# Kernel tuning notes

Hardware: AMD Instinct MI355X
Metric: run time of the kernel (lower is better)

## Reference

```python
import jax, jax.numpy as jnp
import numpy as np

B, S, D, H = 2, 2048, 1024, 16
DK = D // H

def setup_inputs() -> dict:
    key = jax.random.key(0)
    ks = jax.random.split(key, 12)
    scale = 1.0 / np.sqrt(D)
    inp = {
        'q_in': jax.random.normal(ks[0], (B, S, D), jnp.float32),
        'k_in': jax.random.normal(ks[1], (B, S, D), jnp.float32),
        'v_in': jax.random.normal(ks[2], (B, S, D), jnp.float32),
        'mask': jax.random.randint(ks[3], (B, 1, 1, S), 0, 2, jnp.int32),
        'w_q': jax.random.normal(ks[4], (D, D), jnp.float32) * scale,
        'b_q': jnp.zeros((D,), jnp.float32),
        'w_k': jax.random.normal(ks[5], (D, D), jnp.float32) * scale,
        'b_k': jnp.zeros((D,), jnp.float32),
        'w_v': jax.random.normal(ks[6], (D, D), jnp.float32) * scale,
        'b_v': jnp.zeros((D,), jnp.float32),
        'w_o': jax.random.normal(ks[7], (D, D), jnp.float32) * scale,
        'b_o': jnp.zeros((D,), jnp.float32),
    }
    return inp

def _split_heads(x):
    # [B, S, D] -> [B, H, S, DK]
    return x.reshape(B, S, H, DK).transpose(0, 2, 1, 3)

def reference(q_in, k_in, v_in, mask, w_q, b_q, w_k, b_k, w_v, b_v, w_o, b_o):
    q = _split_heads(q_in @ w_q.T + b_q)
    k = _split_heads(k_in @ w_k.T + b_k)
    v = _split_heads(v_in @ w_v.T + b_v)
    scores = jnp.einsum('bhqd,bhkd->bhqk', q, k) / jnp.sqrt(jnp.float32(DK))
    scores = jnp.where(mask == 0, jnp.float32(-1e9), scores)
    attn = jax.nn.softmax(scores, axis=-1)
    ctx = jnp.einsum('bhqk,bhkd->bhqd', attn, v)
    ctx = ctx.transpose(0, 2, 1, 3).reshape(B, S, D)
    return ctx @ w_o.T + b_o
```

## Files before the change

kernel.cpp:

```cpp
#include <hip/hip_runtime.h>
#include <math.h>

#define Bn 2
#define Sn 2048
#define Dn 1024
#define Hn 16
#define DKn 64
#define Mn (Bn*Sn)

typedef __bf16 bf16;
typedef __attribute__((ext_vector_type(8))) __bf16 bf16x8;
typedef __attribute__((ext_vector_type(4))) __bf16 bf16x4;
typedef __attribute__((ext_vector_type(4))) float f32x4;

__device__ inline f32x4 mfma16(bf16x8 a, bf16x8 b, f32x4 c) {
    return __builtin_amdgcn_mfma_f32_16x16x32_bf16(a, b, c, 0, 0, 0);
}

typedef __attribute__((address_space(3))) void lds_t;
typedef const __attribute__((address_space(1))) void gbl_t;
__device__ __forceinline__ void glds16(const void* g, void* l) {
    __builtin_amdgcn_global_load_lds((gbl_t*)g, (lds_t*)l, 16, 0, 0);
}

__global__ __launch_bounds__(256)
void conv3(const float* __restrict__ s0, const float* __restrict__ s1,
           const float* __restrict__ s2, bf16* __restrict__ d0,
           bf16* __restrict__ d1, bf16* __restrict__ d2)
{
    const float* s = blockIdx.y == 0 ? s0 : blockIdx.y == 1 ? s1 : s2;
    bf16*       d = blockIdx.y == 0 ? d0 : blockIdx.y == 1 ? d1 : d2;
    int i = (blockIdx.x * 256 + threadIdx.x) * 8;
    float4 a = *(const float4*)(s + i);
    float4 b = *(const float4*)(s + i + 4);
    bf16x8 o;
    o[0]=(bf16)a.x; o[1]=(bf16)a.y; o[2]=(bf16)a.z; o[3]=(bf16)a.w;
    o[4]=(bf16)b.x; o[5]=(bf16)b.y; o[6]=(bf16)b.z; o[7]=(bf16)b.w;
    *(bf16x8*)(d + i) = o;
}

__global__ __launch_bounds__(256)
void conv_w(const float* __restrict__ s0, const float* __restrict__ s1,
            const float* __restrict__ s2, const float* __restrict__ s3,
            bf16* __restrict__ d0, bf16* __restrict__ d1,
            bf16* __restrict__ d2, bf16* __restrict__ d3)
{
    const float* s = blockIdx.y == 0 ? s0 : blockIdx.y == 1 ? s1 :
                     blockIdx.y == 2 ? s2 : s3;
    bf16*       d = blockIdx.y == 0 ? d0 : blockIdx.y == 1 ? d1 :
                     blockIdx.y == 2 ? d2 : d3;
    int i = (blockIdx.x * 256 + threadIdx.x) * 8;
    float4 a = *(const float4*)(s + i);
    float4 b = *(const float4*)(s + i + 4);
    bf16x8 o;
    o[0]=(bf16)a.x; o[1]=(bf16)a.y; o[2]=(bf16)a.z; o[3]=(bf16)a.w;
    o[4]=(bf16)b.x; o[5]=(bf16)b.y; o[6]=(bf16)b.z; o[7]=(bf16)b.w;
    *(bf16x8*)(d + i) = o;
}

__global__ __launch_bounds__(64)
void mask_scan(const int* __restrict__ mask, int* __restrict__ inv,
               int* __restrict__ cnt)
{
    const int b    = blockIdx.x;
    const int lane = threadIdx.x;
    const int* mb  = mask + b * Sn;
    int loc[32];
    int c = 0;
    #pragma unroll
    for (int e = 0; e < 32; ++e) {
        loc[e] = (mb[lane * 32 + e] != 0) ? 1 : 0;
        c += loc[e];
    }
    int pre = c;
    #pragma unroll
    for (int off = 1; off < 64; off <<= 1) {
        int v = __shfl_up(pre, off);
        if (lane >= off) pre += v;
    }
    int excl  = pre - c;
    int total = __shfl(pre, 63);
    int un = excl;
    int ms = lane * 32 - excl;
    #pragma unroll
    for (int e = 0; e < 32; ++e) {
        int s = lane * 32 + e;
        if (loc[e]) { inv[b * Sn + un] = s;           ++un; }
        else        { inv[b * Sn + total + ms] = s;   ++ms; }
    }
    if (lane == 63) cnt[b] = total;
}

__global__ __launch_bounds__(256)
void gemm_proj(const bf16* __restrict__ Aq, const bf16* __restrict__ Ak,
               const bf16* __restrict__ Av, const bf16* __restrict__ Wq,
               const bf16* __restrict__ Wk, const bf16* __restrict__ Wv,
               const float* __restrict__ bq, const float* __restrict__ bk,
               const float* __restrict__ bv, const int* __restrict__ inv,
               const int* __restrict__ cnt,
               bf16* __restrict__ Cq, bf16* __restrict__ Ck, bf16* __restrict__ Cv)
{
    __shared__ bf16 As[128][32];
    __shared__ bf16 Ws_[128][32];

    const int bid = blockIdx.x;
    const int l   = (bid & 7) * 96 + (bid >> 3);
    const int z   = l >> 8;
    const int rem = l & 255;
    const int mt  = rem >> 3;
    const int n0  = (rem & 7) * 128;
    const int m0  = mt * 128;
    const int bb  = mt >> 4;
    const int s0  = (mt & 15) * 128;

    if (z >= 1) {
        int eff = cnt[bb];
        if (eff == 0) eff = Sn;
        if (s0 >= eff) return;
    }

    const bf16*  A    = z == 0 ? Aq : z == 1 ? Ak : Av;
    const bf16*  W    = z == 0 ? Wq : z == 1 ? Wk : Wv;
    const float* bias = z == 0 ? bq : z == 1 ? bk : bv;
    bf16*        C    = z == 0 ? Cq : z == 1 ? Ck : Cv;

    const int tid = threadIdx.x;
    const int w4 = tid >> 6, ln = tid & 63;
    const int p = ln & 15, g = ln >> 4;
    const int wr = w4 >> 1, wc = w4 & 1;

    const int arow = w4 * 32 + (ln >> 2);
    const int acol = (ln & 3) * 8;

    int row0, row1;
    if (z == 0) { row0 = m0 + arow; row1 = m0 + arow + 16; }
    else {
        row0 = bb * Sn + inv[bb * Sn + s0 + arow];
        row1 = bb * Sn + inv[bb * Sn + s0 + arow + 16];
    }
    const bf16* ga0 = A + (size_t)row0 * Dn + acol;
    const bf16* ga1 = A + (size_t)row1 * Dn + acol;
    const bf16* gw  = W + (size_t)(n0 + arow) * Dn + acol;

    f32x4 acc[4][4];
    #pragma unroll
    for (int mi = 0; mi < 4; ++mi)
        #pragma unroll
        for (int ni = 0; ni < 4; ++ni) acc[mi][ni] = (f32x4){0.f,0.f,0.f,0.f};

    for (int k0 = 0; k0 < Dn; k0 += 32) {
        __syncthreads();
        glds16(ga0 + k0,          &As [w4*32     ][0]);
        glds16(ga1 + k0,          &As [w4*32 + 16][0]);
        glds16(gw  + k0,          &Ws_[w4*32     ][0]);
        glds16(gw  + k0 + 16*Dn,  &Ws_[w4*32 + 16][0]);
        __syncthreads();

        bf16x8 af[4], bfr[4];
        #pragma unroll
        for (int mi = 0; mi < 4; ++mi)
            af[mi] = *(const bf16x8*)&As[wr*64 + mi*16 + p][g*8];
        #pragma unroll
        for (int ni = 0; ni < 4; ++ni)
            bfr[ni] = *(const bf16x8*)&Ws_[wc*64 + ni*16 + p][g*8];
        #pragma unroll
        for (int mi = 0; mi < 4; ++mi)
            #pragma unroll
            for (int ni = 0; ni < 4; ++ni)
                acc[mi][ni] = mfma16(af[mi], bfr[ni], acc[mi][ni]);
    }

    if (z == 0) {
        const float osc = 0.18033688011112042f;
        #pragma unroll
        for (int ni = 0; ni < 4; ++ni) {
            int n = n0 + wc*64 + ni*16 + p;
            int h = n >> 6, dk = n & (DKn - 1);
            float bv = bias[n];
            #pragma unroll
            for (int mi = 0; mi < 4; ++mi)
                #pragma unroll
                for (int r = 0; r < 4; ++r) {
                    int m = m0 + wr*64 + mi*16 + 4*g + r;
                    int b = m >> 11, s = m & (Sn - 1);
                    C[(((size_t)(b*Hn + h)*Sn + s)*DKn) + dk] =
                        (bf16)((acc[mi][ni][r] + bv) * osc);
                }
        }
    } else if (z == 1) {
        #pragma unroll
        for (int ni = 0; ni < 4; ++ni) {
            int n = n0 + wc*64 + ni*16 + p;
            int h = n >> 6, dk = n & (DKn - 1);
            float bv = bias[n];
            #pragma unroll
            for (int mi = 0; mi < 4; ++mi)
                #pragma unroll
                for (int r = 0; r < 4; ++r) {
                    int jj = s0 + wr*64 + mi*16 + 4*g + r;
                    C[(((size_t)(bb*Hn + h)*Sn + jj)*DKn) + dk] =
                        (bf16)(acc[mi][ni][r] + bv);
                }
        }
    } else {
        #pragma unroll
        for (int ni = 0; ni < 4; ++ni) {
            int n = n0 + wc*64 + ni*16 + p;
            int h = n >> 6, dk = n & (DKn - 1);
            float bv = bias[n];
            #pragma unroll
            for (int mi = 0; mi < 4; ++mi)
                #pragma unroll
                for (int r = 0; r < 4; ++r) {
                    int jj = s0 + wr*64 + mi*16 + 4*g + r;
                    C[(((size_t)(bb*Hn + h)*DKn + dk)*Sn) + jj] =
                        (bf16)(acc[mi][ni][r] + bv);
                }
        }
    }
}

__global__ __launch_bounds__(256)
void gemm_out(const bf16* __restrict__ A, const bf16* __restrict__ W,
              const float* __restrict__ bias, float* __restrict__ C)
{
    __shared__ bf16 As[128][32];
    __shared__ bf16 Ws_[64][32];

    const int bid = blockIdx.x;
    const int l   = (bid & 7) * 64 + (bid >> 3);
    const int m0  = (l >> 4) * 128;
    const int n0  = (l & 15) * 64;

    const int tid = threadIdx.x;
    const int w4 = tid >> 6, ln = tid & 63;
    const int p = ln & 15, g = ln >> 4;
    const int wr = w4 >> 1, wc = w4 & 1;

    const int arow = w4 * 32 + (ln >> 2);
    const int acol = (ln & 3) * 8;
    const bf16* ga = A + (size_t)(m0 + arow) * Dn + acol;
    const bf16* gw = W + (size_t)(n0 + w4*16 + (ln >> 2)) * Dn + acol;

    f32x4 acc[4][2];
    #pragma unroll
    for (int mi = 0; mi < 4; ++mi)
        #pragma unroll
        for (int ni = 0; ni < 2; ++ni) acc[mi][ni] = (f32x4){0.f,0.f,0.f,0.f};

    for (int k0 = 0; k0 < Dn; k0 += 32) {
        __syncthreads();
        glds16(ga + k0,          &As [w4*32     ][0]);
        glds16(ga + k0 + 16*Dn,  &As [w4*32 + 16][0]);
        glds16(gw + k0,          &Ws_[w4*16     ][0]);
        __syncthreads();

        bf16x8 af[4], bfr[2];
        #pragma unroll
        for (int mi = 0; mi < 4; ++mi)
            af[mi] = *(const bf16x8*)&As[wr*64 + mi*16 + p][g*8];
        #pragma unroll
        for (int ni = 0; ni < 2; ++ni)
            bfr[ni] = *(const bf16x8*)&Ws_[wc*32 + ni*16 + p][g*8];
        #pragma unroll
        for (int mi = 0; mi < 4; ++mi)
            #pragma unroll
            for (int ni = 0; ni < 2; ++ni)
                acc[mi][ni] = mfma16(af[mi], bfr[ni], acc[mi][ni]);
    }

    #pragma unroll
    for (int ni = 0; ni < 2; ++ni) {
        int n = n0 + wc*32 + ni*16 + p;
        float bv = bias[n];
        #pragma unroll
        for (int mi = 0; mi < 4; ++mi)
            #pragma unroll
            for (int r = 0; r < 4; ++r) {
                int m = m0 + wr*64 + mi*16 + 4*g + r;
                C[(size_t)m * Dn + n] = acc[mi][ni][r] + bv;
            }
    }
}

__global__ __launch_bounds__(512)
void attn_mfma(const bf16* __restrict__ Q, const bf16* __restrict__ K,
               const bf16* __restrict__ Vt, const int* __restrict__ cnt,
               bf16* __restrict__ ctx)
{
    __shared__ bf16 Ks[2][64][64];
    __shared__ bf16 Vs[2][64][64];
    __shared__ bf16 Ps[8][16][72];

    const int tid  = threadIdx.x;
    const int lane = tid & 63;
    const int w    = tid >> 6;
    const int g    = lane >> 4;
    const int p    = lane & 15;
    const int bh   = blockIdx.y;
    const int b    = bh >> 4;
    const int h    = bh & 15;
    const int q0   = blockIdx.x * 128;

    const int  cntb = cnt[b];
    const bool unif = (cntb == 0);
    const int  nt   = unif ? (Sn / 64) : ((cntb + 63) >> 6);

    const bf16* Qb = Q  + (size_t)bh * Sn * DKn;
    const bf16* Kb = K  + (size_t)bh * Sn * DKn;
    const bf16* Vb = Vt + (size_t)bh * DKn * Sn;

    const int sr   = lane >> 3;
    const int scol = 8 * ((lane & 7) ^ sr);
    const int drow = w * 8 + sr;
    const int swzk = (p & 7) << 3;
    const bf16* gK = Kb + (size_t)drow * DKn + scol;
    const bf16* gV = Vb + (size_t)drow * Sn  + scol;

    bf16x8 aq0, aq1;
    {
        const bf16* qrow = Qb + (size_t)(q0 + w*16 + p) * DKn + 8*g;
        aq0 = *(const bf16x8*)(qrow);
        aq1 = *(const bf16x8*)(qrow + 32);
    }

    f32x4 o[4];
    #pragma unroll
    for (int dt = 0; dt < 4; ++dt) o[dt] = (f32x4){0.f,0.f,0.f,0.f};
    float lq = 0.f;

    glds16(gK, &Ks[0][w*8][0]);
    glds16(gV, &Vs[0][w*8][0]);
    __syncthreads();

    int bf = 0;
    for (int kt = 0; kt < nt; ++kt) {
        if (kt + 1 < nt) {
            glds16(gK + (size_t)(kt+1)*64*DKn, &Ks[bf^1][w*8][0]);
            glds16(gV + (size_t)(kt+1)*64,     &Vs[bf^1][w*8][0]);
        }

        const bool tail = (!unif) && (kt == nt - 1);
        const int  rem  = cntb - (kt << 6);

        #pragma unroll
        for (int t = 0; t < 4; ++t) {
            f32x4 z = (f32x4){0.f,0.f,0.f,0.f};
            bf16x8 k0 = *(const bf16x8*)&Ks[bf][16*t + p][(8*g)      ^ swzk];
            bf16x8 k1 = *(const bf16x8*)&Ks[bf][16*t + p][(8*g + 32) ^ swzk];
            z = mfma16(k0, aq0, z);
            z = mfma16(k1, aq1, z);
            bf16x4 pk;
            if (unif) {
                pk[0] = (bf16)1.f; pk[1] = (bf16)1.f;
                pk[2] = (bf16)1.f; pk[3] = (bf16)1.f;
                lq += 4.f;
            } else if (tail) {
                int kb = 16*t + 4*g;
                pk[0] = (bf16)(kb + 0 < rem ? exp2f(z[0]) : 0.f);
                pk[1] = (bf16)(kb + 1 < rem ? exp2f(z[1]) : 0.f);
                pk[2] = (bf16)(kb + 2 < rem ? exp2f(z[2]) : 0.f);
                pk[3] = (bf16)(kb + 3 < rem ? exp2f(z[3]) : 0.f);
                lq += (float)pk[0] + (float)pk[1] + (float)pk[2] + (float)pk[3];
            } else {
                pk[0] = (bf16)exp2f(z[0]);
                pk[1] = (bf16)exp2f(z[1]);
                pk[2] = (bf16)exp2f(z[2]);
                pk[3] = (bf16)exp2f(z[3]);
                lq += (float)pk[0] + (float)pk[1] + (float)pk[2] + (float)pk[3];
            }
            *(bf16x4*)&Ps[w][p][16*t + 4*g] = pk;
        }

        bf16x8 pa0 = *(const bf16x8*)&Ps[w][p][8*g];
        bf16x8 pa1 = *(const bf16x8*)&Ps[w][p][32 + 8*g];
        #pragma unroll
        for (int dt = 0; dt < 4; ++dt) {
            bf16x8 v0 = *(const bf16x8*)&Vs[bf][16*dt + p][(8*g)      ^ swzk];
            bf16x8 v1 = *(const bf16x8*)&Vs[bf][16*dt + p][(8*g + 32) ^ swzk];
            o[dt] = mfma16(pa0, v0, o[dt]);
            o[dt] = mfma16(pa1, v1, o[dt]);
        }

        __syncthreads();
        bf ^= 1;
    }

    lq += __shfl_xor(lq, 16);
    lq += __shfl_xor(lq, 32);
    float ld[4];
    #pragma unroll
    for (int r = 0; r < 4; ++r) ld[r] = __shfl(lq, 4*g + r);

    #pragma unroll
    for (int dt = 0; dt < 4; ++dt)
        #pragma unroll
        for (int r = 0; r < 4; ++r) {
            int s_ = q0 + w*16 + 4*g + r;
            ctx[(size_t)(b*Sn + s_) * Dn + h*64 + 16*dt + p] =
                (bf16)(o[dt][r] / ld[r]);
        }
}

extern "C" void kernel_launch(void* const* d_in, const int* in_sizes, int n_in,
                              void* d_out, int out_size, void* d_ws, size_t ws_size,
                              hipStream_t stream) {
    const float* q_in = (const float*)d_in[0];
    const float* k_in = (const float*)d_in[1];
    const float* v_in = (const float*)d_in[2];
    const int*   mask = (const int*)  d_in[3];
    const float* w_q  = (const float*)d_in[4];
    const float* b_q  = (const float*)d_in[5];
    const float* w_k  = (const float*)d_in[6];
    const float* b_k  = (const float*)d_in[7];
    const float* w_v  = (const float*)d_in[8];
    const float* b_v  = (const float*)d_in[9];
    const float* w_o  = (const float*)d_in[10];
    const float* b_o  = (const float*)d_in[11];

    char* ws = (char*)d_ws;
    bf16* Abf_q = (bf16*)(ws);
    bf16* Abf_k = (bf16*)(ws + 8388608);
    bf16* Abf_v = (bf16*)(ws + 16777216);
    bf16* ctx   = (bf16*)(ws);
    bf16* Qh    = (bf16*)(ws + 25165824);
    bf16* Kh    = (bf16*)(ws + 33554432);
    bf16* Vt    = (bf16*)(ws + 41943040);
    bf16* Wbf_q = (bf16*)(ws + 50331648);
    bf16* Wbf_k = (bf16*)(ws + 52428800);
    bf16* Wbf_v = (bf16*)(ws + 54525952);
    bf16* Wbf_o = (bf16*)(ws + 56623104);
    int*  inv   = (int*) (ws + 58720256);
    int*  cntb  = (int*) (ws + 58736640);

    dim3 blk(256);
    conv3<<<dim3(2048, 3), blk, 0, stream>>>(q_in, k_in, v_in, Abf_q, Abf_k, Abf_v);
    conv_w<<<dim3(512, 4), blk, 0, stream>>>(w_q, w_k, w_v, w_o,
                                             Wbf_q, Wbf_k, Wbf_v, Wbf_o);
    mask_scan<<<dim3(Bn), dim3(64), 0, stream>>>(mask, inv, cntb);

    gemm_proj<<<dim3(768), blk, 0, stream>>>(
        Abf_q, Abf_k, Abf_v, Wbf_q, Wbf_k, Wbf_v, b_q, b_k, b_v, inv, cntb,
        Qh, Kh, Vt);

    attn_mfma<<<dim3(Sn/128, Bn*Hn), dim3(512), 0, stream>>>(Qh, Kh, Vt, cntb, ctx);

    gemm_out<<<dim3(512), blk, 0, stream>>>(ctx, Wbf_o, b_o, (float*)d_out);
}
```

Measured before the change: 125.2 us.

## Fuse prep kernels into one launch and use K=64 swizzled LDS tiles in GEMMs

The three preprocessing kernels (activation conversion, weight conversion, mask scan) are merged into a single launch, removing two kernel launches and their gaps. Both projection GEMMs now stage 64-wide K slices per iteration instead of 32, halving the number of barrier pairs per K loop. An XOR swizzle on the 16-byte column chunk is added to spread LDS accesses across banks. The doubled LDS footprint per block may reduce occupancy, and the mask-scan blocks leave most of their threads idle.

```diff
diff --git a/kernel.cpp b/kernel.cpp
--- a/kernel.cpp
+++ b/kernel.cpp
@@ -24,71 +24,65 @@
 }
 
 __global__ __launch_bounds__(256)
-void conv3(const float* __restrict__ s0, const float* __restrict__ s1,
-           const float* __restrict__ s2, bf16* __restrict__ d0,
-           bf16* __restrict__ d1, bf16* __restrict__ d2)
+void prep(const float* __restrict__ q_in, const float* __restrict__ k_in,
+          const float* __restrict__ v_in, const float* __restrict__ w_q,
+          const float* __restrict__ w_k, const float* __restrict__ w_v,
+          const float* __restrict__ w_o, const int* __restrict__ mask,
+          bf16* __restrict__ Aq, bf16* __restrict__ Ak, bf16* __restrict__ Av,
+          bf16* __restrict__ Wq, bf16* __restrict__ Wk, bf16* __restrict__ Wv,
+          bf16* __restrict__ Wo, int* __restrict__ inv, int* __restrict__ cnt)
 {
-    const float* s = blockIdx.y == 0 ? s0 : blockIdx.y == 1 ? s1 : s2;
-    bf16*       d = blockIdx.y == 0 ? d0 : blockIdx.y == 1 ? d1 : d2;
-    int i = (blockIdx.x * 256 + threadIdx.x) * 8;
-    float4 a = *(const float4*)(s + i);
-    float4 b = *(const float4*)(s + i + 4);
-    bf16x8 o;
-    o[0]=(bf16)a.x; o[1]=(bf16)a.y; o[2]=(bf16)a.z; o[3]=(bf16)a.w;
-    o[4]=(bf16)b.x; o[5]=(bf16)b.y; o[6]=(bf16)b.z; o[7]=(bf16)b.w;
-    *(bf16x8*)(d + i) = o;
-}
-
-__global__ __launch_bounds__(256)
-void conv_w(const float* __restrict__ s0, const float* __restrict__ s1,
-            const float* __restrict__ s2, const float* __restrict__ s3,
-            bf16* __restrict__ d0, bf16* __restrict__ d1,
-            bf16* __restrict__ d2, bf16* __restrict__ d3)
-{
-    const float* s = blockIdx.y == 0 ? s0 : blockIdx.y == 1 ? s1 :
-                     blockIdx.y == 2 ? s2 : s3;
-    bf16*       d = blockIdx.y == 0 ? d0 : blockIdx.y == 1 ? d1 :
-                     blockIdx.y == 2 ? d2 : d3;
-    int i = (blockIdx.x * 256 + threadIdx.x) * 8;
-    float4 a = *(const float4*)(s + i);
-    float4 b = *(const float4*)(s + i + 4);
-    bf16x8 o;
-    o[0]=(bf16)a.x; o[1]=(bf16)a.y; o[2]=(bf16)a.z; o[3]=(bf16)a.w;
-    o[4]=(bf16)b.x; o[5]=(bf16)b.y; o[6]=(bf16)b.z; o[7]=(bf16)b.w;
-    *(bf16x8*)(d + i) = o;
-}
-
-__global__ __launch_bounds__(64)
-void mask_scan(const int* __restrict__ mask, int* __restrict__ inv,
-               int* __restrict__ cnt)
-{
-    const int b    = blockIdx.x;
-    const int lane = threadIdx.x;
-    const int* mb  = mask + b * Sn;
-    int loc[32];
-    int c = 0;
-    #pragma unroll
-    for (int e = 0; e < 32; ++e) {
-        loc[e] = (mb[lane * 32 + e] != 0) ? 1 : 0;
-        c += loc[e];
-    }
-    int pre = c;
-    #pragma unroll
-    for (int off = 1; off < 64; off <<= 1) {
-        int v = __shfl_up(pre, off);
-        if (lane >= off) pre += v;
-    }
-    int excl  = pre - c;
-    int total = __shfl(pre, 63);
-    int un = excl;
-    int ms = lane * 32 - excl;
-    #pragma unroll
-    for (int e = 0; e < 32; ++e) {
-        int s = lane * 32 + e;
-        if (loc[e]) { inv[b * Sn + un] = s;           ++un; }
-        else        { inv[b * Sn + total + ms] = s;   ++ms; }
-    }
-    if (lane == 63) cnt[b] = total;
+    const int bid = blockIdx.x;
+    if (bid < 8192) {
+        const float* s; bf16* d; int i;
+        if (bid < 6144) {
+            int y = bid / 2048, x = bid - y * 2048;
+            s = y == 0 ? q_in : y == 1 ? k_in : v_in;
+            d = y == 0 ? Aq   : y == 1 ? Ak   : Av;
+            i = (x * 256 + threadIdx.x) * 8;
+        } else {
+            int r = bid - 6144;
+            int y = r / 512, x = r - y * 512;
+            s = y == 0 ? w_q : y == 1 ? w_k : y == 2 ? w_v : w_o;
+            d = y == 0 ? Wq  : y == 1 ? Wk  : y == 2 ? Wv  : Wo;
+            i = (x * 256 + threadIdx.x) * 8;
+        }
+        float4 a = *(const float4*)(s + i);
+        float4 b = *(const float4*)(s + i + 4);
+        bf16x8 o;
+        o[0]=(bf16)a.x; o[1]=(bf16)a.y; o[2]=(bf16)a.z; o[3]=(bf16)a.w;
+        o[4]=(bf16)b.x; o[5]=(bf16)b.y; o[6]=(bf16)b.z; o[7]=(bf16)b.w;
+        *(bf16x8*)(d + i) = o;
+    } else {
+        if (threadIdx.x >= 64) return;
+        const int b    = bid - 8192;
+        const int lane = threadIdx.x;
+        const int* mb  = mask + b * Sn;
+        int loc[32];
+        int c = 0;
+        #pragma unroll
+        for (int e = 0; e < 32; ++e) {
+            loc[e] = (mb[lane * 32 + e] != 0) ? 1 : 0;
+            c += loc[e];
+        }
+        int pre = c;
+        #pragma unroll
+        for (int off = 1; off < 64; off <<= 1) {
+            int v = __shfl_up(pre, off);
+            if (lane >= off) pre += v;
+        }
+        int excl  = pre - c;
+        int total = __shfl(pre, 63);
+        int un = excl;
+        int ms = lane * 32 - excl;
+        #pragma unroll
+        for (int e = 0; e < 32; ++e) {
+            int s = lane * 32 + e;
+            if (loc[e]) { inv[b * Sn + un] = s;           ++un; }
+            else        { inv[b * Sn + total + ms] = s;   ++ms; }
+        }
+        if (lane == 63) cnt[b] = total;
+    }
 }
 
 __global__ __launch_bounds__(256)
@@ -100,8 +94,8 @@
                const int* __restrict__ cnt,
                bf16* __restrict__ Cq, bf16* __restrict__ Ck, bf16* __restrict__ Cv)
 {
-    __shared__ bf16 As[128][32];
-    __shared__ bf16 Ws_[128][32];
+    __shared__ bf16 As[128][64];
+    __shared__ bf16 Ws_[128][64];
 
     const int bid = blockIdx.x;
     const int l   = (bid & 7) * 96 + (bid >> 3);
@@ -129,18 +123,21 @@
     const int p = ln & 15, g = ln >> 4;
     const int wr = w4 >> 1, wc = w4 & 1;
 
-    const int arow = w4 * 32 + (ln >> 2);
-    const int acol = (ln & 3) * 8;
-
-    int row0, row1;
-    if (z == 0) { row0 = m0 + arow; row1 = m0 + arow + 16; }
-    else {
-        row0 = bb * Sn + inv[bb * Sn + s0 + arow];
-        row1 = bb * Sn + inv[bb * Sn + s0 + arow + 16];
-    }
-    const bf16* ga0 = A + (size_t)row0 * Dn + acol;
-    const bf16* ga1 = A + (size_t)row1 * Dn + acol;
-    const bf16* gw  = W + (size_t)(n0 + arow) * Dn + acol;
+    const int lr   = ln >> 3;
+    const int scol = 8 * ((ln & 7) ^ lr);
+    const int sw   = p & 7;
+
+    const bf16* ga[4];
+    const bf16* gw[4];
+    #pragma unroll
+    for (int i = 0; i < 4; ++i) {
+        int lrow = w4*32 + i*8 + lr;
+        int row;
+        if (z == 0) row = m0 + lrow;
+        else        row = bb * Sn + inv[bb * Sn + s0 + lrow];
+        ga[i] = A + (size_t)row * Dn + scol;
+        gw[i] = W + (size_t)(n0 + lrow) * Dn + scol;
+    }
 
     f32x4 acc[4][4];
     #pragma unroll
@@ -148,26 +145,32 @@
         #pragma unroll
         for (int ni = 0; ni < 4; ++ni) acc[mi][ni] = (f32x4){0.f,0.f,0.f,0.f};
 
-    for (int k0 = 0; k0 < Dn; k0 += 32) {
+    for (int k0 = 0; k0 < Dn; k0 += 64) {
         __syncthreads();
-        glds16(ga0 + k0,          &As [w4*32     ][0]);
-        glds16(ga1 + k0,          &As [w4*32 + 16][0]);
-        glds16(gw  + k0,          &Ws_[w4*32     ][0]);
-        glds16(gw  + k0 + 16*Dn,  &Ws_[w4*32 + 16][0]);
+        #pragma unroll
+        for (int i = 0; i < 4; ++i) {
+            glds16(ga[i] + k0, &As [w4*32 + i*8][0]);
+            glds16(gw[i] + k0, &Ws_[w4*32 + i*8][0]);
+        }
         __syncthreads();
 
-        bf16x8 af[4], bfr[4];
-        #pragma unroll
-        for (int mi = 0; mi < 4; ++mi)
-            af[mi] = *(const bf16x8*)&As[wr*64 + mi*16 + p][g*8];
-        #pragma unroll
-        for (int ni = 0; ni < 4; ++ni)
-            bfr[ni] = *(const bf16x8*)&Ws_[wc*64 + ni*16 + p][g*8];
-        #pragma unroll
-        for (int mi = 0; mi < 4; ++mi)
+        #pragma unroll
+        for (int kk = 0; kk < 2; ++kk) {
+            bf16x8 af[4], bfr[4];
+            #pragma unroll
+            for (int mi = 0; mi < 4; ++mi)
+                af[mi] = *(const bf16x8*)
+                    &As[wr*64 + mi*16 + p][8 * ((g + 4*kk) ^ sw)];
             #pragma unroll
             for (int ni = 0; ni < 4; ++ni)
-                acc[mi][ni] = mfma16(af[mi], bfr[ni], acc[mi][ni]);
+                bfr[ni] = *(const bf16x8*)
+                    &Ws_[wc*64 + ni*16 + p][8 * ((g + 4*kk) ^ sw)];
+            #pragma unroll
+            for (int mi = 0; mi < 4; ++mi)
+                #pragma unroll
+                for (int ni = 0; ni < 4; ++ni)
+                    acc[mi][ni] = mfma16(af[mi], bfr[ni], acc[mi][ni]);
+        }
     }
 
     if (z == 0) {
@@ -224,8 +227,8 @@
 void gemm_out(const bf16* __restrict__ A, const bf16* __restrict__ W,
               const float* __restrict__ bias, float* __restrict__ C)
 {
-    __shared__ bf16 As[128][32];
-    __shared__ bf16 Ws_[64][32];
+    __shared__ bf16 As[128][64];
+    __shared__ bf16 Ws_[64][64];
 
     const int bid = blockIdx.x;
     const int l   = (bid & 7) * 64 + (bid >> 3);
@@ -237,10 +240,18 @@
     const int p = ln & 15, g = ln >> 4;
     const int wr = w4 >> 1, wc = w4 & 1;
 
-    const int arow = w4 * 32 + (ln >> 2);
-    const int acol = (ln & 3) * 8;
-    const bf16* ga = A + (size_t)(m0 + arow) * Dn + acol;
-    const bf16* gw = W + (size_t)(n0 + w4*16 + (ln >> 2)) * Dn + acol;
+    const int lr   = ln >> 3;
+    const int scol = 8 * ((ln & 7) ^ lr);
+    const int sw   = p & 7;
+
+    const bf16* ga[4];
+    const bf16* gw[2];
+    #pragma unroll
+    for (int i = 0; i < 4; ++i)
+        ga[i] = A + (size_t)(m0 + w4*32 + i*8 + lr) * Dn + scol;
+    #pragma unroll
+    for (int i = 0; i < 2; ++i)
+        gw[i] = W + (size_t)(n0 + w4*16 + i*8 + lr) * Dn + scol;
 
     f32x4 acc[4][2];
     #pragma unroll
@@ -248,25 +259,33 @@
         #pragma unroll
         for (int ni = 0; ni < 2; ++ni) acc[mi][ni] = (f32x4){0.f,0.f,0.f,0.f};
 
-    for (int k0 = 0; k0 < Dn; k0 += 32) {
+    for (int k0 = 0; k0 < Dn; k0 += 64) {
         __syncthreads();
-        glds16(ga + k0,          &As [w4*32     ][0]);
-        glds16(ga + k0 + 16*Dn,  &As [w4*32 + 16][0]);
-        glds16(gw + k0,          &Ws_[w4*16     ][0]);
+        #pragma unroll
+        for (int i = 0; i < 4; ++i)
+            glds16(ga[i] + k0, &As[w4*32 + i*8][0]);
+        #pragma unroll
+        for (int i = 0; i < 2; ++i)
+            glds16(gw[i] + k0, &Ws_[w4*16 + i*8][0]);
         __syncthreads();
 
-        bf16x8 af[4], bfr[2];
-        #pragma unroll
-        for (int mi = 0; mi < 4; ++mi)
-            af[mi] = *(const bf16x8*)&As[wr*64 + mi*16 + p][g*8];
-        #pragma unroll
-        for (int ni = 0; ni < 2; ++ni)
-            bfr[ni] = *(const bf16x8*)&Ws_[wc*32 + ni*16 + p][g*8];
-        #pragma unroll
-        for (int mi = 0; mi < 4; ++mi)
+        #pragma unroll
+        for (int kk = 0; kk < 2; ++kk) {
+            bf16x8 af[4], bfr[2];
+            #pragma unroll
+            for (int mi = 0; mi < 4; ++mi)
+                af[mi] = *(const bf16x8*)
+                    &As[wr*64 + mi*16 + p][8 * ((g + 4*kk) ^ sw)];
             #pragma unroll
             for (int ni = 0; ni < 2; ++ni)
-                acc[mi][ni] = mfma16(af[mi], bfr[ni], acc[mi][ni]);
+                bfr[ni] = *(const bf16x8*)
+                    &Ws_[wc*32 + ni*16 + p][8 * ((g + 4*kk) ^ sw)];
+            #pragma unroll
+            for (int mi = 0; mi < 4; ++mi)
+                #pragma unroll
+                for (int ni = 0; ni < 2; ++ni)
+                    acc[mi][ni] = mfma16(af[mi], bfr[ni], acc[mi][ni]);
+        }
     }
 
     #pragma unroll
@@ -434,10 +453,9 @@
     int*  cntb  = (int*) (ws + 58736640);
 
     dim3 blk(256);
-    conv3<<<dim3(2048, 3), blk, 0, stream>>>(q_in, k_in, v_in, Abf_q, Abf_k, Abf_v);
-    conv_w<<<dim3(512, 4), blk, 0, stream>>>(w_q, w_k, w_v, w_o,
-                                             Wbf_q, Wbf_k, Wbf_v, Wbf_o);
-    mask_scan<<<dim3(Bn), dim3(64), 0, stream>>>(mask, inv, cntb);
+    prep<<<dim3(8194), blk, 0, stream>>>(q_in, k_in, v_in, w_q, w_k, w_v, w_o,
+                                         mask, Abf_q, Abf_k, Abf_v,
+                                         Wbf_q, Wbf_k, Wbf_v, Wbf_o, inv, cntb);
 
     gemm_proj<<<dim3(768), blk, 0, stream>>>(
         Abf_q, Abf_k, Abf_v, Wbf_q, Wbf_k, Wbf_v, b_q, b_k, b_v, inv, cntb,
```

Measured after the change: 112.5 us. 10.1% less time.
